# Kernel optimization log

Hardware: AMD Instinct MI355X
Metric: run time of the kernel (lower is better)

## Reference

```python
import jax, jax.numpy as jnp
import numpy as np

WS = 8          # window size -> N = 64
SHIFT = 4       # shift size for shifted windows
FEAT = 32       # feature map H = W at stage 3
C = 512         # channels (SwinV2-B stage 3)
HEADS = 16
B_IMG = 128     # images -> 128 * (32/8)^2 = 2048 windows


def _rel_coords_table():
    # log-spaced continuous relative coords table, SwinV2 style: [(2W-1)^2, 2]
    r = np.arange(-(WS - 1), WS, dtype=np.float32)
    t = np.stack(np.meshgrid(r, r, indexing='ij'), axis=-1)  # [15,15,2]
    t = t / (WS - 1) * 8.0
    t = np.sign(t) * np.log2(np.abs(t) + 1.0) / np.log2(8.0)
    return t.reshape(-1, 2)


def _rel_pos_index():
    c = np.stack(np.meshgrid(np.arange(WS), np.arange(WS), indexing='ij'))  # [2,8,8]
    cf = c.reshape(2, -1)
    rel = (cf[:, :, None] - cf[:, None, :]).transpose(1, 2, 0)  # [64,64,2]
    rel[:, :, 0] += WS - 1
    rel[:, :, 1] += WS - 1
    rel[:, :, 0] *= 2 * WS - 1
    return rel.sum(-1).astype(np.int32)  # [64,64]


def _shift_mask():
    # standard SwinV2 shifted-window attention mask: [nW, N, N] in {0, -100}
    img = np.zeros((FEAT, FEAT), dtype=np.float32)
    cnt = 0
    for hs in (slice(0, -WS), slice(-WS, -SHIFT), slice(-SHIFT, None)):
        for ws in (slice(0, -WS), slice(-WS, -SHIFT), slice(-SHIFT, None)):
            img[hs, ws] = cnt
            cnt += 1
    win = img.reshape(FEAT // WS, WS, FEAT // WS, WS).transpose(0, 2, 1, 3)
    win = win.reshape(-1, WS * WS)  # [nW, 64]
    diff = win[:, None, :] - win[:, :, None]
    return np.where(diff != 0, -100.0, 0.0).astype(np.float32)


def setup_inputs() -> dict:
    key = jax.random.key(0)
    ks = jax.random.split(key, 10)
    nW = (FEAT // WS) ** 2  # 16 windows per image
    Bw = B_IMG * nW         # 2048
    N = WS * WS
    s = 0.02
    return {
        'x': jax.random.normal(ks[0], (Bw, N, C), jnp.float32),
        'mask': jnp.asarray(_shift_mask()),
        'qkv_w': jax.random.normal(ks[1], (3 * C, C), jnp.float32) * s,
        'q_bias': jnp.zeros((C,), jnp.float32),
        'v_bias': jnp.zeros((C,), jnp.float32),
        'logit_scale': jnp.full((HEADS, 1, 1), np.log(10.0), jnp.float32),
        'cpb_w1': jax.random.normal(ks[2], (512, 2), jnp.float32) * s,
        'cpb_b1': jnp.zeros((512,), jnp.float32),
        'cpb_w2': jax.random.normal(ks[3], (HEADS, 512), jnp.float32) * s,
        'proj_w': jax.random.normal(ks[4], (C, C), jnp.float32) * s,
        'proj_b': jnp.zeros((C,), jnp.float32),
        'rel_coords_table': jnp.asarray(_rel_coords_table()),
        'rel_pos_index': jnp.asarray(_rel_pos_index()),
    }


def reference(x, mask, qkv_w, q_bias, v_bias, logit_scale, cpb_w1, cpb_b1,
              cpb_w2, proj_w, proj_b, rel_coords_table, rel_pos_index):
    Bw, N, Cdim = x.shape
    H = logit_scale.shape[0]
    d = Cdim // H
    # qkv projection; k has no bias (SwinV2)
    qkv_bias = jnp.concatenate([q_bias, jnp.zeros_like(q_bias), v_bias])
    qkv = (x @ qkv_w.T + qkv_bias).reshape(Bw, N, 3, H, d).transpose(2, 0, 3, 1, 4)
    q, k, v = qkv[0], qkv[1], qkv[2]  # each [Bw,H,N,d]
    # cosine attention with learned per-head temperature
    qn = q / jnp.maximum(jnp.linalg.norm(q, axis=-1, keepdims=True), 1e-12)
    kn = k / jnp.maximum(jnp.linalg.norm(k, axis=-1, keepdims=True), 1e-12)
    attn = jnp.einsum('bhnd,bhmd->bhnm', qn, kn)
    scale = jnp.exp(jnp.minimum(logit_scale, jnp.log(100.0)))  # [H,1,1]
    attn = attn * scale[None]
    # continuous relative position bias via small MLP over log-spaced coords
    tbl = jax.nn.relu(rel_coords_table @ cpb_w1.T + cpb_b1) @ cpb_w2.T  # [(2W-1)^2,H]
    bias = tbl[rel_pos_index.reshape(-1)].reshape(N, N, H).transpose(2, 0, 1)
    attn = attn + 16.0 * jax.nn.sigmoid(bias)[None]
    # shifted-window mask applied per window group
    nW = mask.shape[0]
    attn = attn.reshape(Bw // nW, nW, H, N, N) + mask[None, :, None]
    attn = jax.nn.softmax(attn.reshape(Bw, H, N, N), axis=-1)
    out = jnp.einsum('bhnm,bhmd->bhnd', attn, v)
    out = out.transpose(0, 2, 1, 3).reshape(Bw, N, Cdim)
    return out @ proj_w.T + proj_b
```

## Files before the change

### kernel.cpp

```cpp
#include <hip/hip_runtime.h>
#include <stdint.h>
#include <stddef.h>


typedef __attribute__((ext_vector_type(8))) short bf16x8;
typedef __attribute__((ext_vector_type(4))) float f32x4;
typedef __attribute__((ext_vector_type(4))) unsigned short us4;
typedef __attribute__((ext_vector_type(8))) unsigned short us8;
typedef unsigned short u16;
typedef unsigned int u32;

__device__ __forceinline__ u16 f2bf(float f) {
  union { __bf16 b; u16 u; } cv;
  cv.b = (__bf16)f;
  return cv.u;
}
__device__ __forceinline__ float bf2f(u16 s) {
  return __uint_as_float(((u32)s) << 16);
}
__device__ __forceinline__ void gl_lds16(const void* g, void* l) {
  __builtin_amdgcn_global_load_lds(
      (const __attribute__((address_space(1))) u32*)g,
      (__attribute__((address_space(3))) u32*)l, 16, 0, 0);
}
__device__ __forceinline__ f32x4 mfma16(bf16x8 a, bf16x8 b, f32x4 c) {
  return __builtin_amdgcn_mfma_f32_16x16x32_bf16(a, b, c, 0, 0, 0);
}


__global__ void conv_w_kernel(const float* __restrict__ QW, const float* __restrict__ PW,
                              u16* __restrict__ WQB, u16* __restrict__ WPB) {
  int idx = blockIdx.x * 256 + threadIdx.x;
  const int NQ = 1536 * 512 / 4;
  float4 v; u16* dst;
  if (idx < NQ) { v = ((const float4*)QW)[idx]; dst = WQB + (size_t)idx * 4; }
  else { int k = idx - NQ; v = ((const float4*)PW)[k]; dst = WPB + (size_t)k * 4; }
  us4 u; u.x = f2bf(v.x); u.y = f2bf(v.y); u.z = f2bf(v.z); u.w = f2bf(v.w);
  *(us4*)dst = u;
}

__global__ void sig16_kernel(const float* __restrict__ CT, const float* __restrict__ W1,
                             const float* __restrict__ B1, const float* __restrict__ W2,
                             float* __restrict__ SIG) {
  int i = blockIdx.x;
  int tid = threadIdx.x;
  float c0 = CT[i * 2 + 0], c1 = CT[i * 2 + 1];
  float a[16];
  #pragma unroll
  for (int hh = 0; hh < 16; ++hh) a[hh] = 0.f;
  #pragma unroll
  for (int jj = 0; jj < 2; ++jj) {
    int j = tid + jj * 256;
    float h = fmaxf(c0 * W1[j * 2 + 0] + c1 * W1[j * 2 + 1] + B1[j], 0.f);
    #pragma unroll
    for (int hh = 0; hh < 16; ++hh) a[hh] += h * W2[hh * 512 + j];
  }
  __shared__ float red[4][16];
  #pragma unroll
  for (int hh = 0; hh < 16; ++hh) {
    float v = a[hh];
    for (int m = 1; m < 64; m <<= 1) v += __shfl_xor(v, m);
    if ((tid & 63) == 0) red[tid >> 6][hh] = v;
  }
  __syncthreads();
  if (tid < 16) {
    float v = red[0][tid] + red[1][tid] + red[2][tid] + red[3][tid];
    SIG[i * 16 + tid] = 16.f / (1.f + __expf(-v));
  }
}

__global__ void cmb_kernel(const float* __restrict__ SIG, const float* __restrict__ MASK,
                           const int* __restrict__ RPI, float* __restrict__ CMB) {
  int b = blockIdx.x;
  int w = b >> 4, h = b & 15;
  int tid = threadIdx.x;
  const float* mrow = &MASK[(size_t)w * 4096];
  float* crow = &CMB[(size_t)b * 4096];
  #pragma unroll
  for (int it = 0; it < 16; ++it) {
    int nm = it * 256 + tid;
    crow[nm] = SIG[RPI[nm] * 16 + h] + mrow[nm];
  }
}


__global__ __launch_bounds__(256, 2) void qkv_gemm(
    const float* __restrict__ X, const u16* __restrict__ WB,
    const float* __restrict__ QB, const float* __restrict__ VB,
    u16* __restrict__ QKV) {
  __shared__ u16 As[128 * 64];
  __shared__ u16 Bs[128 * 64];
  const int tid = threadIdx.x, lane = tid & 63, w = tid >> 6;
  int bid = blockIdx.x;
  int swz = (bid & 7) * 1536 + (bid >> 3);
  const int mt = swz / 12, nt = swz - mt * 12;
  const long m0 = (long)mt * 128, n0 = (long)nt * 128;
  const int wm = w >> 1, wn = w & 1;
  const f32x4 zf = {0.f, 0.f, 0.f, 0.f};

  f32x4 acc[4][4];
  #pragma unroll
  for (int mi = 0; mi < 4; ++mi)
    #pragma unroll
    for (int ni = 0; ni < 4; ++ni) acc[mi][ni] = zf;

  const u16* Ap = &As[(wm * 64 + (lane & 15)) * 64 + ((lane >> 4) * 8)];
  const u16* Bp = &Bs[(wn * 64 + (lane & 15)) * 64 + ((lane >> 4) * 8)];

  for (int t = 0; t < 8; ++t) {
    float4 av[8];
    #pragma unroll
    for (int i = 0; i < 8; ++i) {
      int ch = tid + (i << 8);
      int row = ch >> 4, kc = ch & 15;
      av[i] = *(const float4*)&X[(m0 + row) * 512 + t * 64 + kc * 4];
    }
    #pragma unroll
    for (int i = 0; i < 4; ++i) {
      int ch = ((w << 2) + i) * 64 + lane;
      int row = ch >> 3, kc = ch & 7;
      gl_lds16(&WB[(n0 + row) * 512 + t * 64 + kc * 8], &Bs[((w << 2) + i) * 512]);
    }
    #pragma unroll
    for (int i = 0; i < 8; ++i) {
      int ch = tid + (i << 8);
      int row = ch >> 4, kc = ch & 15;
      us4 u; u.x = f2bf(av[i].x); u.y = f2bf(av[i].y); u.z = f2bf(av[i].z); u.w = f2bf(av[i].w);
      *(us4*)&As[row * 64 + kc * 4] = u;
    }
    __syncthreads();
    #pragma unroll
    for (int ks = 0; ks < 2; ++ks) {
      bf16x8 af[4], bfr[4];
      #pragma unroll
      for (int mi = 0; mi < 4; ++mi) af[mi] = *(const bf16x8*)&Ap[mi * 1024 + ks * 32];
      #pragma unroll
      for (int ni = 0; ni < 4; ++ni) bfr[ni] = *(const bf16x8*)&Bp[ni * 1024 + ks * 32];
      #pragma unroll
      for (int mi = 0; mi < 4; ++mi)
        #pragma unroll
        for (int ni = 0; ni < 4; ++ni)
          acc[mi][ni] = mfma16(af[mi], bfr[ni], acc[mi][ni]);
    }
    __syncthreads();
  }

  #pragma unroll
  for (int ni = 0; ni < 4; ++ni) {
    const long c = n0 + wn * 64 + ni * 16 + (lane & 15);
    float bias = (c < 512) ? QB[c] : (c < 1024 ? 0.f : VB[c - 1024]);
    #pragma unroll
    for (int mi = 0; mi < 4; ++mi)
      #pragma unroll
      for (int r = 0; r < 4; ++r) {
        long row = m0 + wm * 64 + mi * 16 + (lane >> 4) * 4 + r;
        QKV[row * 1536 + c] = f2bf(acc[mi][ni][r] + bias);
      }
  }
}


__global__ __launch_bounds__(256, 4) void attn_kernel(
    u16* __restrict__ QKV, const float* __restrict__ CMB, const float* __restrict__ LS) {
  __shared__ u16 sm[7424];
  u16* qs = sm;
  u16* ksm = sm + 2560;
  u16* ps = sm;
  u16* vt = sm + 5120;
  const int tid = threadIdx.x, lane = tid & 63, w = tid >> 6;
  const int b = blockIdx.x, wi = b & 15;
  const size_t base = (size_t)b * 64 * 1536;
  const int cl = lane & 15, lg = lane >> 4;
  const int srow = tid >> 2, sck = tid & 3;
  const int vd = tid & 31, vkb = tid >> 5;
  const f32x4 zf = {0.f, 0.f, 0.f, 0.f};

  for (int h = 0; h < 16; ++h) {
    const float scale = __expf(fminf(LS[h], 4.6051702f));
    {
      us8 qv = *(const us8*)&QKV[base + (size_t)srow * 1536 + h * 32 + sck * 8];
      float qf[8]; float ss = 0.f;
      #pragma unroll
      for (int j = 0; j < 8; ++j) { qf[j] = bf2f(qv[j]); ss += qf[j] * qf[j]; }
      ss += __shfl_xor(ss, 1); ss += __shfl_xor(ss, 2);
      float rn = scale / fmaxf(sqrtf(ss), 1e-12f);
      us8 qo;
      #pragma unroll
      for (int j = 0; j < 8; ++j) qo[j] = f2bf(qf[j] * rn);
      *(us8*)&qs[srow * 40 + sck * 8] = qo;
    }
    {
      us8 kv = *(const us8*)&QKV[base + (size_t)srow * 1536 + 512 + h * 32 + sck * 8];
      float kf[8]; float ss = 0.f;
      #pragma unroll
      for (int j = 0; j < 8; ++j) { kf[j] = bf2f(kv[j]); ss += kf[j] * kf[j]; }
      ss += __shfl_xor(ss, 1); ss += __shfl_xor(ss, 2);
      float rn = 1.f / fmaxf(sqrtf(ss), 1e-12f);
      us8 ko;
      #pragma unroll
      for (int j = 0; j < 8; ++j) ko[j] = f2bf(kf[j] * rn);
      *(us8*)&ksm[srow * 40 + sck * 8] = ko;
    }
    {
      us8 vo;
      #pragma unroll
      for (int e = 0; e < 8; ++e)
        vo[e] = QKV[base + (size_t)(vkb * 8 + e) * 1536 + 1024 + h * 32 + vd];
      *(us8*)&vt[vd * 72 + vkb * 8] = vo;
    }
    __syncthreads();

    bf16x8 aq = *(const bf16x8*)&qs[(w * 16 + cl) * 40 + lg * 8];
    f32x4 s4[4];
    #pragma unroll
    for (int nt = 0; nt < 4; ++nt) {
      bf16x8 bk = *(const bf16x8*)&ksm[(nt * 16 + cl) * 40 + lg * 8];
      s4[nt] = mfma16(aq, bk, zf);
    }

    const float* cp = &CMB[((size_t)(wi * 16 + h)) << 12];
    const int r0 = w * 16 + lg * 4;
    float p[4][4];
    #pragma unroll
    for (int r = 0; r < 4; ++r) {
      float mx = -3.0e38f;
      #pragma unroll
      for (int q4 = 0; q4 < 4; ++q4) {
        float v = s4[q4][r] + cp[(r0 + r) * 64 + q4 * 16 + cl];
        p[q4][r] = v; mx = fmaxf(mx, v);
      }
      mx = fmaxf(mx, __shfl_xor(mx, 1));
      mx = fmaxf(mx, __shfl_xor(mx, 2));
      mx = fmaxf(mx, __shfl_xor(mx, 4));
      mx = fmaxf(mx, __shfl_xor(mx, 8));
      float sum = 0.f;
      #pragma unroll
      for (int q4 = 0; q4 < 4; ++q4) { float e = __expf(p[q4][r] - mx); p[q4][r] = e; sum += e; }
      sum += __shfl_xor(sum, 1); sum += __shfl_xor(sum, 2);
      sum += __shfl_xor(sum, 4); sum += __shfl_xor(sum, 8);
      float inv = 1.f / sum;
      #pragma unroll
      for (int q4 = 0; q4 < 4; ++q4) p[q4][r] *= inv;
    }
    __syncthreads();

    #pragma unroll
    for (int r = 0; r < 4; ++r)
      #pragma unroll
      for (int q4 = 0; q4 < 4; ++q4)
        ps[(r0 + r) * 72 + q4 * 16 + cl] = f2bf(p[q4][r]);

    f32x4 o4[2]; o4[0] = zf; o4[1] = zf;
    #pragma unroll
    for (int ks = 0; ks < 2; ++ks) {
      bf16x8 ap = *(const bf16x8*)&ps[(w * 16 + cl) * 72 + ks * 32 + lg * 8];
      #pragma unroll
      for (int n2 = 0; n2 < 2; ++n2) {
        bf16x8 bv = *(const bf16x8*)&vt[(n2 * 16 + cl) * 72 + ks * 32 + lg * 8];
        o4[n2] = mfma16(ap, bv, o4[n2]);
      }
    }
    #pragma unroll
    for (int n2 = 0; n2 < 2; ++n2)
      #pragma unroll
      for (int r = 0; r < 4; ++r)
        QKV[base + (size_t)(w * 16 + lg * 4 + r) * 1536 + h * 32 + n2 * 16 + cl] = f2bf(o4[n2][r]);
    __syncthreads();
  }
}


__global__ __launch_bounds__(256, 2) void proj_gemm(
    const u16* __restrict__ A, const u16* __restrict__ WB,
    const float* __restrict__ PB, float* __restrict__ OUT) {
  __shared__ u16 As[128 * 64];
  __shared__ u16 Bs[128 * 64];
  const int tid = threadIdx.x, lane = tid & 63, w = tid >> 6;
  int bid = blockIdx.x;
  int swz = (bid & 7) * 512 + (bid >> 3);
  const int mt = swz >> 2, nt = swz & 3;
  const long m0 = (long)mt * 128, n0 = (long)nt * 128;
  const int wm = w >> 1, wn = w & 1;
  const f32x4 zf = {0.f, 0.f, 0.f, 0.f};

  f32x4 acc[4][4];
  #pragma unroll
  for (int mi = 0; mi < 4; ++mi)
    #pragma unroll
    for (int ni = 0; ni < 4; ++ni) acc[mi][ni] = zf;

  const u16* Ap = &As[(wm * 64 + (lane & 15)) * 64 + ((lane >> 4) * 8)];
  const u16* Bp = &Bs[(wn * 64 + (lane & 15)) * 64 + ((lane >> 4) * 8)];

  for (int t = 0; t < 8; ++t) {
    #pragma unroll
    for (int i = 0; i < 4; ++i) {
      int ch = ((w << 2) + i) * 64 + lane;
      int row = ch >> 3, kc = ch & 7;
      gl_lds16(&A[(m0 + row) * 1536 + t * 64 + kc * 8], &As[((w << 2) + i) * 512]);
      gl_lds16(&WB[(n0 + row) * 512 + t * 64 + kc * 8], &Bs[((w << 2) + i) * 512]);
    }
    __syncthreads();
    #pragma unroll
    for (int ks = 0; ks < 2; ++ks) {
      bf16x8 af[4], bfr[4];
      #pragma unroll
      for (int mi = 0; mi < 4; ++mi) af[mi] = *(const bf16x8*)&Ap[mi * 1024 + ks * 32];
      #pragma unroll
      for (int ni = 0; ni < 4; ++ni) bfr[ni] = *(const bf16x8*)&Bp[ni * 1024 + ks * 32];
      #pragma unroll
      for (int mi = 0; mi < 4; ++mi)
        #pragma unroll
        for (int ni = 0; ni < 4; ++ni)
          acc[mi][ni] = mfma16(af[mi], bfr[ni], acc[mi][ni]);
    }
    __syncthreads();
  }

  #pragma unroll
  for (int ni = 0; ni < 4; ++ni) {
    const long c = n0 + wn * 64 + ni * 16 + (lane & 15);
    float bias = PB[c];
    #pragma unroll
    for (int mi = 0; mi < 4; ++mi)
      #pragma unroll
      for (int r = 0; r < 4; ++r) {
        long row = m0 + wm * 64 + mi * 16 + (lane >> 4) * 4 + r;
        OUT[row * 512 + c] = acc[mi][ni][r] + bias;
      }
  }
}


extern "C" void kernel_launch(void* const* d_in, const int* in_sizes, int n_in,
                              void* d_out, int out_size, void* d_ws, size_t ws_size,
                              hipStream_t stream) {
  const float* X    = (const float*)d_in[0];
  const float* MASK = (const float*)d_in[1];
  const float* QW   = (const float*)d_in[2];
  const float* QB   = (const float*)d_in[3];
  const float* VB   = (const float*)d_in[4];
  const float* LS   = (const float*)d_in[5];
  const float* CW1  = (const float*)d_in[6];
  const float* CB1  = (const float*)d_in[7];
  const float* CW2  = (const float*)d_in[8];
  const float* PW   = (const float*)d_in[9];
  const float* PB   = (const float*)d_in[10];
  const float* CT   = (const float*)d_in[11];
  const int*   RPI  = (const int*)d_in[12];
  float* OUT = (float*)d_out;

  char* ws = (char*)d_ws;
  u16*   QKV = (u16*)ws;
  float* CMB = (float*)(ws + 402653184ull);
  float* SIG = (float*)(ws + 406847488ull);
  u16*   WQB = (u16*)(ws + 406861888ull);
  u16*   WPB = (u16*)(ws + 408434752ull);

  conv_w_kernel<<<1024, 256, 0, stream>>>(QW, PW, WQB, WPB);
  sig16_kernel<<<225, 256, 0, stream>>>(CT, CW1, CB1, CW2, SIG);
  cmb_kernel<<<256, 256, 0, stream>>>(SIG, MASK, RPI, CMB);
  qkv_gemm<<<12288, 256, 0, stream>>>(X, WQB, QB, VB, QKV);
  attn_kernel<<<2048, 256, 0, stream>>>(QKV, CMB, LS);
  proj_gemm<<<4096, 256, 0, stream>>>(QKV, WPB, PB, OUT);
}
```

Measured before the change: 732.5 us.

## Rewrite QKV and proj GEMMs as 256x256 double-buffered swizzled-LDS pipelines

```diff
diff --git a/kernel.cpp b/kernel.cpp
--- a/kernel.cpp
+++ b/kernel.cpp
@@ -9,6 +9,10 @@
 typedef __attribute__((ext_vector_type(8))) unsigned short us8;
 typedef unsigned short u16;
 typedef unsigned int u32;
+
+#define FENCE() asm volatile("" ::: "memory")
+#define WAITV0() asm volatile("s_waitcnt vmcnt(0)" ::: "memory")
+#define WAITL0() asm volatile("s_waitcnt lgkmcnt(0)" ::: "memory")
 
 __device__ __forceinline__ u16 f2bf(float f) {
   union { __bf16 b; u16 u; } cv;
@@ -84,76 +88,106 @@
 }
 
 
-__global__ __launch_bounds__(256, 2) void qkv_gemm(
+__global__ __launch_bounds__(512, 1) void qkv_gemm(
     const float* __restrict__ X, const u16* __restrict__ WB,
     const float* __restrict__ QB, const float* __restrict__ VB,
     u16* __restrict__ QKV) {
-  __shared__ u16 As[128 * 64];
-  __shared__ u16 Bs[128 * 64];
+  __shared__ u16 S[65536];
   const int tid = threadIdx.x, lane = tid & 63, w = tid >> 6;
   int bid = blockIdx.x;
-  int swz = (bid & 7) * 1536 + (bid >> 3);
-  const int mt = swz / 12, nt = swz - mt * 12;
-  const long m0 = (long)mt * 128, n0 = (long)nt * 128;
-  const int wm = w >> 1, wn = w & 1;
+  int swz = (bid & 7) * 384 + (bid >> 3);
+  const int mt = swz / 6, nt = swz - mt * 6;
+  const long m0 = (long)mt * 256, n0 = (long)nt * 256;
+  const int wm = w >> 2, wn = w & 3;
+  const int fr = lane & 15;
+  const int fsw = ((lane >> 4) ^ (lane & 7)) << 3;
+  const int akc = tid & 15, arow = tid >> 4;
   const f32x4 zf = {0.f, 0.f, 0.f, 0.f};
 
-  f32x4 acc[4][4];
-  #pragma unroll
-  for (int mi = 0; mi < 4; ++mi)
+  f32x4 acc[8][4];
+  #pragma unroll
+  for (int mi = 0; mi < 8; ++mi)
     #pragma unroll
     for (int ni = 0; ni < 4; ++ni) acc[mi][ni] = zf;
 
-  const u16* Ap = &As[(wm * 64 + (lane & 15)) * 64 + ((lane >> 4) * 8)];
-  const u16* Bp = &Bs[(wn * 64 + (lane & 15)) * 64 + ((lane >> 4) * 8)];
+  float4 av[8];
+  auto loadA = [&](int kt) {
+    #pragma unroll
+    for (int i = 0; i < 8; ++i)
+      av[i] = *(const float4*)&X[(m0 + i * 32 + arow) * 512 + kt * 64 + akc * 4];
+  };
+  auto writeA = [&](int kt) {
+    u16* dst = &S[(kt & 1) * 32768];
+    #pragma unroll
+    for (int i = 0; i < 8; ++i) {
+      int row = i * 32 + arow;
+      us4 u; u.x = f2bf(av[i].x); u.y = f2bf(av[i].y); u.z = f2bf(av[i].z); u.w = f2bf(av[i].w);
+      *(us4*)&dst[row * 64 + (((akc >> 1) ^ (row & 7)) << 3) + ((akc & 1) << 2)] = u;
+    }
+  };
+  auto stageB = [&](int kt, int p) {
+    u16* dst = &S[(kt & 1) * 32768 + 16384 + p * 8192];
+    #pragma unroll
+    for (int i = 0; i < 2; ++i) {
+      int ch = i * 512 + w * 64 + lane;
+      int row = ch >> 3, kcs = (ch & 7) ^ (row & 7);
+      gl_lds16(&WB[(size_t)(n0 + p * 128 + row) * 512 + kt * 64 + kcs * 8],
+               &dst[(i * 512 + w * 64) * 8]);
+    }
+  };
+
+  loadA(0); stageB(0, 0); stageB(0, 1);
+  WAITV0(); writeA(0); WAITL0();
+  FENCE(); __builtin_amdgcn_s_barrier(); FENCE();
 
   for (int t = 0; t < 8; ++t) {
-    float4 av[8];
-    #pragma unroll
-    for (int i = 0; i < 8; ++i) {
-      int ch = tid + (i << 8);
-      int row = ch >> 4, kc = ch & 15;
-      av[i] = *(const float4*)&X[(m0 + row) * 512 + t * 64 + kc * 4];
-    }
-    #pragma unroll
-    for (int i = 0; i < 4; ++i) {
-      int ch = ((w << 2) + i) * 64 + lane;
-      int row = ch >> 3, kc = ch & 7;
-      gl_lds16(&WB[(n0 + row) * 512 + t * 64 + kc * 8], &Bs[((w << 2) + i) * 512]);
-    }
-    #pragma unroll
-    for (int i = 0; i < 8; ++i) {
-      int ch = tid + (i << 8);
-      int row = ch >> 4, kc = ch & 15;
-      us4 u; u.x = f2bf(av[i].x); u.y = f2bf(av[i].y); u.z = f2bf(av[i].z); u.w = f2bf(av[i].w);
-      *(us4*)&As[row * 64 + kc * 4] = u;
-    }
-    __syncthreads();
-    #pragma unroll
-    for (int ks = 0; ks < 2; ++ks) {
-      bf16x8 af[4], bfr[4];
-      #pragma unroll
-      for (int mi = 0; mi < 4; ++mi) af[mi] = *(const bf16x8*)&Ap[mi * 1024 + ks * 32];
-      #pragma unroll
-      for (int ni = 0; ni < 4; ++ni) bfr[ni] = *(const bf16x8*)&Bp[ni * 1024 + ks * 32];
-      #pragma unroll
-      for (int mi = 0; mi < 4; ++mi)
+    const u16* As_ = &S[(t & 1) * 32768];
+    const u16* Bs_ = As_ + 16384;
+    #pragma unroll
+    for (int q = 0; q < 4; ++q) {
+      const int qm = q >> 1, qn = q & 1;
+      bf16x8 af0[4], af1[4], bv0[2], bv1[2];
+      #pragma unroll
+      for (int m = 0; m < 4; ++m) {
+        const u16* p = As_ + (wm * 128 + (qm * 4 + m) * 16 + fr) * 64 + fsw;
+        af0[m] = *(const bf16x8*)p;
+        af1[m] = *(const bf16x8*)((const u16*)((uintptr_t)p ^ 64));
+      }
+      #pragma unroll
+      for (int n = 0; n < 2; ++n) {
+        const u16* p = Bs_ + (wn * 64 + (qn * 2 + n) * 16 + fr) * 64 + fsw;
+        bv0[n] = *(const bf16x8*)p;
+        bv1[n] = *(const bf16x8*)((const u16*)((uintptr_t)p ^ 64));
+      }
+      if (t < 7) {
+        if (q == 0) loadA(t + 1);
+        else if (q == 1) stageB(t + 1, 0);
+        else if (q == 2) stageB(t + 1, 1);
+      }
+      FENCE(); __builtin_amdgcn_s_barrier(); FENCE();
+      __builtin_amdgcn_s_setprio(1);
+      #pragma unroll
+      for (int m = 0; m < 4; ++m)
         #pragma unroll
-        for (int ni = 0; ni < 4; ++ni)
-          acc[mi][ni] = mfma16(af[mi], bfr[ni], acc[mi][ni]);
-    }
-    __syncthreads();
+        for (int n = 0; n < 2; ++n) {
+          acc[qm * 4 + m][qn * 2 + n] = mfma16(af0[m], bv0[n], acc[qm * 4 + m][qn * 2 + n]);
+          acc[qm * 4 + m][qn * 2 + n] = mfma16(af1[m], bv1[n], acc[qm * 4 + m][qn * 2 + n]);
+        }
+      __builtin_amdgcn_s_setprio(0);
+      if (q == 3 && t < 7) { WAITV0(); writeA(t + 1); WAITL0(); }
+      FENCE(); __builtin_amdgcn_s_barrier(); FENCE();
+    }
   }
 
   #pragma unroll
   for (int ni = 0; ni < 4; ++ni) {
-    const long c = n0 + wn * 64 + ni * 16 + (lane & 15);
+    const long c = n0 + wn * 64 + ni * 16 + fr;
     float bias = (c < 512) ? QB[c] : (c < 1024 ? 0.f : VB[c - 1024]);
     #pragma unroll
-    for (int mi = 0; mi < 4; ++mi)
+    for (int mi = 0; mi < 8; ++mi)
       #pragma unroll
       for (int r = 0; r < 4; ++r) {
-        long row = m0 + wm * 64 + mi * 16 + (lane >> 4) * 4 + r;
+        long row = m0 + wm * 128 + mi * 16 + (lane >> 4) * 4 + r;
         QKV[row * 1536 + c] = f2bf(acc[mi][ni][r] + bias);
       }
   }
@@ -270,62 +304,100 @@
 }
 
 
-__global__ __launch_bounds__(256, 2) void proj_gemm(
+__global__ __launch_bounds__(512, 1) void proj_gemm(
     const u16* __restrict__ A, const u16* __restrict__ WB,
     const float* __restrict__ PB, float* __restrict__ OUT) {
-  __shared__ u16 As[128 * 64];
-  __shared__ u16 Bs[128 * 64];
+  __shared__ u16 S[65536];
   const int tid = threadIdx.x, lane = tid & 63, w = tid >> 6;
   int bid = blockIdx.x;
-  int swz = (bid & 7) * 512 + (bid >> 3);
-  const int mt = swz >> 2, nt = swz & 3;
-  const long m0 = (long)mt * 128, n0 = (long)nt * 128;
-  const int wm = w >> 1, wn = w & 1;
+  int swz = (bid & 7) * 128 + (bid >> 3);
+  const int mt = swz >> 1, nt = swz & 1;
+  const long m0 = (long)mt * 256, n0 = (long)nt * 256;
+  const int wm = w >> 2, wn = w & 3;
+  const int fr = lane & 15;
+  const int fsw = ((lane >> 4) ^ (lane & 7)) << 3;
   const f32x4 zf = {0.f, 0.f, 0.f, 0.f};
 
-  f32x4 acc[4][4];
-  #pragma unroll
-  for (int mi = 0; mi < 4; ++mi)
+  f32x4 acc[8][4];
+  #pragma unroll
+  for (int mi = 0; mi < 8; ++mi)
     #pragma unroll
     for (int ni = 0; ni < 4; ++ni) acc[mi][ni] = zf;
 
-  const u16* Ap = &As[(wm * 64 + (lane & 15)) * 64 + ((lane >> 4) * 8)];
-  const u16* Bp = &Bs[(wn * 64 + (lane & 15)) * 64 + ((lane >> 4) * 8)];
+  auto stageA = [&](int kt, int p) {
+    u16* dst = &S[(kt & 1) * 32768 + p * 8192];
+    #pragma unroll
+    for (int i = 0; i < 2; ++i) {
+      int ch = i * 512 + w * 64 + lane;
+      int row = ch >> 3, kcs = (ch & 7) ^ (row & 7);
+      gl_lds16(&A[(size_t)(m0 + p * 128 + row) * 1536 + kt * 64 + kcs * 8],
+               &dst[(i * 512 + w * 64) * 8]);
+    }
+  };
+  auto stageB = [&](int kt, int p) {
+    u16* dst = &S[(kt & 1) * 32768 + 16384 + p * 8192];
+    #pragma unroll
+    for (int i = 0; i < 2; ++i) {
+      int ch = i * 512 + w * 64 + lane;
+      int row = ch >> 3, kcs = (ch & 7) ^ (row & 7);
+      gl_lds16(&WB[(size_t)(n0 + p * 128 + row) * 512 + kt * 64 + kcs * 8],
+               &dst[(i * 512 + w * 64) * 8]);
+    }
+  };
+
+  stageA(0, 0); stageA(0, 1); stageB(0, 0); stageB(0, 1);
+  WAITV0();
+  FENCE(); __builtin_amdgcn_s_barrier(); FENCE();
 
   for (int t = 0; t < 8; ++t) {
-    #pragma unroll
-    for (int i = 0; i < 4; ++i) {
-      int ch = ((w << 2) + i) * 64 + lane;
-      int row = ch >> 3, kc = ch & 7;
-      gl_lds16(&A[(m0 + row) * 1536 + t * 64 + kc * 8], &As[((w << 2) + i) * 512]);
-      gl_lds16(&WB[(n0 + row) * 512 + t * 64 + kc * 8], &Bs[((w << 2) + i) * 512]);
-    }
-    __syncthreads();
-    #pragma unroll
-    for (int ks = 0; ks < 2; ++ks) {
-      bf16x8 af[4], bfr[4];
-      #pragma unroll
-      for (int mi = 0; mi < 4; ++mi) af[mi] = *(const bf16x8*)&Ap[mi * 1024 + ks * 32];
-      #pragma unroll
-      for (int ni = 0; ni < 4; ++ni) bfr[ni] = *(const bf16x8*)&Bp[ni * 1024 + ks * 32];
-      #pragma unroll
-      for (int mi = 0; mi < 4; ++mi)
+    const u16* As_ = &S[(t & 1) * 32768];
+    const u16* Bs_ = As_ + 16384;
+    #pragma unroll
+    for (int q = 0; q < 4; ++q) {
+      const int qm = q >> 1, qn = q & 1;
+      bf16x8 af0[4], af1[4], bv0[2], bv1[2];
+      #pragma unroll
+      for (int m = 0; m < 4; ++m) {
+        const u16* p = As_ + (wm * 128 + (qm * 4 + m) * 16 + fr) * 64 + fsw;
+        af0[m] = *(const bf16x8*)p;
+        af1[m] = *(const bf16x8*)((const u16*)((uintptr_t)p ^ 64));
+      }
+      #pragma unroll
+      for (int n = 0; n < 2; ++n) {
+        const u16* p = Bs_ + (wn * 64 + (qn * 2 + n) * 16 + fr) * 64 + fsw;
+        bv0[n] = *(const bf16x8*)p;
+        bv1[n] = *(const bf16x8*)((const u16*)((uintptr_t)p ^ 64));
+      }
+      if (t < 7) {
+        if (q == 0) stageA(t + 1, 0);
+        else if (q == 1) stageA(t + 1, 1);
+        else if (q == 2) stageB(t + 1, 0);
+        else stageB(t + 1, 1);
+      }
+      FENCE(); __builtin_amdgcn_s_barrier(); FENCE();
+      __builtin_amdgcn_s_setprio(1);
+      #pragma unroll
+      for (int m = 0; m < 4; ++m)
         #pragma unroll
-        for (int ni = 0; ni < 4; ++ni)
-          acc[mi][ni] = mfma16(af[mi], bfr[ni], acc[mi][ni]);
-    }
-    __syncthreads();
+        for (int n = 0; n < 2; ++n) {
+          acc[qm * 4 + m][qn * 2 + n] = mfma16(af0[m], bv0[n], acc[qm * 4 + m][qn * 2 + n]);
+          acc[qm * 4 + m][qn * 2 + n] = mfma16(af1[m], bv1[n], acc[qm * 4 + m][qn * 2 + n]);
+        }
+      __builtin_amdgcn_s_setprio(0);
+      if (q == 3 && t < 7) { WAITV0(); }
+      FENCE(); __builtin_amdgcn_s_barrier(); FENCE();
+    }
   }
 
   #pragma unroll
   for (int ni = 0; ni < 4; ++ni) {
-    const long c = n0 + wn * 64 + ni * 16 + (lane & 15);
+    const long c = n0 + wn * 64 + ni * 16 + fr;
     float bias = PB[c];
     #pragma unroll
-    for (int mi = 0; mi < 4; ++mi)
+    for (int mi = 0; mi < 8; ++mi)
       #pragma unroll
       for (int r = 0; r < 4; ++r) {
-        long row = m0 + wm * 64 + mi * 16 + (lane >> 4) * 4 + r;
+        long row = m0 + wm * 128 + mi * 16 + (lane >> 4) * 4 + r;
         OUT[row * 512 + c] = acc[mi][ni][r] + bias;
       }
   }
@@ -360,7 +432,7 @@
   conv_w_kernel<<<1024, 256, 0, stream>>>(QW, PW, WQB, WPB);
   sig16_kernel<<<225, 256, 0, stream>>>(CT, CW1, CB1, CW2, SIG);
   cmb_kernel<<<256, 256, 0, stream>>>(SIG, MASK, RPI, CMB);
-  qkv_gemm<<<12288, 256, 0, stream>>>(X, WQB, QB, VB, QKV);
+  qkv_gemm<<<3072, 512, 0, stream>>>(X, WQB, QB, VB, QKV);
   attn_kernel<<<2048, 256, 0, stream>>>(QKV, CMB, LS);
-  proj_gemm<<<4096, 256, 0, stream>>>(QKV, WPB, PB, OUT);
-}
+  proj_gemm<<<1024, 512, 0, stream>>>(QKV, WPB, PB, OUT);
+}
```

After: 911.7 us. +24.5%, slower.
